# Performance work log

Hardware: AMD Instinct MI355X
Metric: run time of the kernel (lower is better)

Reference implementation:

```python
import jax, jax.numpy as jnp
import numpy as np

B, I, D = 2048, 20000, 512  # batch, nr_items, embedding_dim
EPS = 1e-12  # tf.nn.l2_normalize epsilon


def setup_inputs() -> dict:
    key = jax.random.key(0)
    ks = jax.random.split(key, 16)
    g = lambda k, shape, fan_in: jax.random.normal(k, shape, jnp.float32) * (1.0 / np.sqrt(fan_in))
    likes = (jax.random.uniform(ks[0], (B, I)) < 0.05).astype(jnp.float32)
    noise_mask = jax.random.uniform(ks[1], (B, I)) < 0.3
    users = jax.random.randint(ks[2], (B,), 0, 100000)
    return {
        'users': users, 'likes': likes, 'noise_mask': noise_mask,
        # encoder: I -> 2D (relu) -> D (relu)
        'enc_w1': g(ks[3], (I, 2 * D), I), 'enc_b1': jnp.zeros((2 * D,), jnp.float32),
        'enc_w2': g(ks[4], (2 * D, D), 2 * D), 'enc_b2': jnp.zeros((D,), jnp.float32),
        # likes_estimator: D -> 2D (relu) -> I (sigmoid)
        'lk_w1': g(ks[5], (D, 2 * D), D), 'lk_b1': jnp.zeros((2 * D,), jnp.float32),
        'lk_w2': g(ks[6], (2 * D, I), 2 * D), 'lk_b2': jnp.zeros((I,), jnp.float32),
        # rec_estimator: D -> 2D (relu) -> I (sigmoid)
        'rc_w1': g(ks[7], (D, 2 * D), D), 'rc_b1': jnp.zeros((2 * D,), jnp.float32),
        'rc_w2': g(ks[8], (2 * D, I), 2 * D), 'rc_b2': jnp.zeros((I,), jnp.float32),
    }


def reference(users, likes, noise_mask, enc_w1, enc_b1, enc_w2, enc_b2,
              lk_w1, lk_b1, lk_w2, lk_b2, rc_w1, rc_b1, rc_w2, rc_b2):
    noisy_likes = jnp.where(noise_mask, 0.0, likes)
    # encoder MLP
    h = jax.nn.relu(noisy_likes @ enc_w1 + enc_b1)
    embed_user = jax.nn.relu(h @ enc_w2 + enc_b2)          # [B, D]
    # heads
    estimated_likes = jax.nn.sigmoid(jax.nn.relu(embed_user @ lk_w1 + lk_b1) @ lk_w2 + lk_b2)
    estimated_rec = jax.nn.sigmoid(jax.nn.relu(embed_user @ rc_w1 + rc_b1) @ rc_w2 + rc_b2)
    # all-pairs cosine similarity as a Gram matrix (no NxNxD tile).
    # tf.keras.losses.cosine_similarity returns the NEGATIVE cosine similarity.
    normed = embed_user * jax.lax.rsqrt(
        jnp.maximum(jnp.sum(embed_user * embed_user, axis=-1, keepdims=True), EPS))
    user_sim = -(normed @ normed.T)                        # [B, B]
    popular = jnp.mean(likes, axis=0)                      # [I]
    return (estimated_likes, user_sim, estimated_rec, popular)
```

## Files before the change

kernel.cpp:

```cpp
#include <hip/hip_runtime.h>
#include <cstdint>
#include <cstddef>

#define B_DIM 2048
#define I_DIM 20000
#define D_DIM 512
#define H_DIM 1024

typedef __bf16 bf16x8 __attribute__((ext_vector_type(8)));
typedef float f32x4 __attribute__((ext_vector_type(4)));

__device__ __forceinline__ unsigned short f2bf(float f) {
  union { float f; unsigned u; } v; v.f = f;
  unsigned u = v.u;
  u += 0x7fffu + ((u >> 16) & 1u);
  return (unsigned short)(u >> 16);
}
__device__ __forceinline__ float bf2f(unsigned short h) {
  union { unsigned u; float f; } v; v.u = ((unsigned)h) << 16;
  return v.f;
}

__device__ __forceinline__ void glds16(const unsigned short* g, unsigned short* l) {
  __builtin_amdgcn_global_load_lds(
      (const __attribute__((address_space(1))) void*)g,
      (__attribute__((address_space(3))) void*)l, 16, 0, 0);
}

__global__ void noisy_popular_kernel(const float* __restrict__ likes,
                                     const int* __restrict__ mask,
                                     unsigned short* __restrict__ noisy,
                                     float* __restrict__ pop) {
  int idx4 = blockIdx.x * 256 + threadIdx.x;
  if (idx4 >= I_DIM / 4) return;
  int r0 = blockIdx.y * 64;
  float4 s = make_float4(0.f, 0.f, 0.f, 0.f);
  for (int r = 0; r < 64; ++r) {
    size_t off = (size_t)(r0 + r) * (I_DIM / 4) + idx4;
    float4 L = ((const float4*)likes)[off];
    int4 M = ((const int4*)mask)[off];
    s.x += L.x; s.y += L.y; s.z += L.z; s.w += L.w;
    ushort4 o;
    o.x = M.x ? (unsigned short)0 : f2bf(L.x);
    o.y = M.y ? (unsigned short)0 : f2bf(L.y);
    o.z = M.z ? (unsigned short)0 : f2bf(L.z);
    o.w = M.w ? (unsigned short)0 : f2bf(L.w);
    ((ushort4*)noisy)[off] = o;
  }
  const float inv = 1.0f / B_DIM;
  atomicAdd(&pop[idx4 * 4 + 0], s.x * inv);
  atomicAdd(&pop[idx4 * 4 + 1], s.y * inv);
  atomicAdd(&pop[idx4 * 4 + 2], s.z * inv);
  atomicAdd(&pop[idx4 * 4 + 3], s.w * inv);
}

__global__ void transpose_to_bf16(const float* __restrict__ in,
                                  unsigned short* __restrict__ out, int R, int C) {
  __shared__ unsigned short tile[32][33];
  int c0 = blockIdx.x * 32, r0 = blockIdx.y * 32;
  int tx = threadIdx.x, ty = threadIdx.y;
#pragma unroll
  for (int i = 0; i < 4; i++) {
    int r = r0 + ty + i * 8;
    tile[ty + i * 8][tx] = f2bf(in[(size_t)r * C + c0 + tx]);
  }
  __syncthreads();
#pragma unroll
  for (int i = 0; i < 4; i++) {
    int c = c0 + ty + i * 8;
    out[(size_t)c * R + r0 + tx] = tile[tx][ty + i * 8];
  }
}

__global__ void concat_bias_kernel(const float* __restrict__ a,
                                   const float* __restrict__ b,
                                   float* __restrict__ out) {
  int i = blockIdx.x * 256 + threadIdx.x;
  if (i < H_DIM) out[i] = a[i];
  else if (i < 2 * H_DIM) out[i] = b[i - H_DIM];
}

__global__ void reduce_relu_kernel(const float* __restrict__ partial,
                                   const float* __restrict__ bias,
                                   unsigned short* __restrict__ h1) {
  int idx4 = blockIdx.x * 256 + threadIdx.x;
  const size_t slice = (size_t)B_DIM * H_DIM / 4;
  float4 s = ((const float4*)partial)[idx4];
#pragma unroll
  for (int z = 1; z < 5; z++) {
    float4 p = ((const float4*)partial)[z * slice + idx4];
    s.x += p.x; s.y += p.y; s.z += p.z; s.w += p.w;
  }
  float4 b = ((const float4*)bias)[idx4 & (H_DIM / 4 - 1)];
  ushort4 o;
  o.x = f2bf(fmaxf(s.x + b.x, 0.f));
  o.y = f2bf(fmaxf(s.y + b.y, 0.f));
  o.z = f2bf(fmaxf(s.z + b.z, 0.f));
  o.w = f2bf(fmaxf(s.w + b.w, 0.f));
  ((ushort4*)h1)[idx4] = o;
}

__global__ void l2norm_kernel(const unsigned short* __restrict__ embed,
                              unsigned short* __restrict__ normed) {
  int row = blockIdx.x * 4 + (threadIdx.x >> 6);
  int lane = threadIdx.x & 63;
  const unsigned short* e = embed + (size_t)row * D_DIM;
  float v[8];
  float ss = 0.f;
#pragma unroll
  for (int j = 0; j < 8; j++) { v[j] = bf2f(e[lane + j * 64]); ss += v[j] * v[j]; }
#pragma unroll
  for (int o = 32; o > 0; o >>= 1) ss += __shfl_xor(ss, o, 64);
  float s = rsqrtf(fmaxf(ss, 1e-12f));
  unsigned short* nr = normed + (size_t)row * D_DIM;
#pragma unroll
  for (int j = 0; j < 8; j++) nr[lane + j * 64] = f2bf(v[j] * s);
}

template <int ACT, bool OBF16>
__global__ __launch_bounds__(256) void gemm128(
    const unsigned short* __restrict__ A, const unsigned short* __restrict__ BT,
    const float* __restrict__ bias, void* __restrict__ Cout,
    int N, int lda, int ldb, int ldc, int kLen, long long zStride) {
  __shared__ unsigned short As[128 * 32];
  __shared__ unsigned short Bs[128 * 32];
  const int n0 = blockIdx.x * 128;
  const int m0 = blockIdx.y * 128;
  const int t = threadIdx.x;
  const int lane = t & 63;
  const int wv = t >> 6;
  const int quad = lane >> 4;
  const int tc = lane & 15;
  const int wm = (wv >> 1) * 64;
  const int wn = (wv & 1) * 64;
  const int k0 = blockIdx.z * kLen;

  f32x4 acc[4][4];
#pragma unroll
  for (int i = 0; i < 4; i++)
#pragma unroll
    for (int j = 0; j < 4; j++) acc[i][j] = (f32x4){0.f, 0.f, 0.f, 0.f};

  const int srow = lane >> 2;
  const int skch = (lane & 3) * 8;
  const unsigned short* gA0 = A + (size_t)(m0 + wv * 32 + srow) * lda + k0 + skch;
  const unsigned short* gA1 = gA0 + (size_t)16 * lda;
  const unsigned short* gB0 = BT + (size_t)(n0 + wv * 32 + srow) * ldb + k0 + skch;
  const unsigned short* gB1 = gB0 + (size_t)16 * ldb;
  unsigned short* lA = As + wv * 1024;
  unsigned short* lB = Bs + wv * 1024;

  const int nIter = kLen >> 5;
  for (int it = 0; it < nIter; ++it) {
    __syncthreads();
    glds16(gA0, lA);
    glds16(gA1, lA + 512);
    glds16(gB0, lB);
    glds16(gB1, lB + 512);
    gA0 += 32; gA1 += 32; gB0 += 32; gB1 += 32;
    __syncthreads();
    bf16x8 a[4], b[4];
#pragma unroll
    for (int i = 0; i < 4; i++) {
      a[i] = *(const bf16x8*)&As[(wm + i * 16 + tc) * 32 + quad * 8];
      b[i] = *(const bf16x8*)&Bs[(wn + i * 16 + tc) * 32 + quad * 8];
    }
#pragma unroll
    for (int i = 0; i < 4; i++)
#pragma unroll
      for (int j = 0; j < 4; j++)
        acc[i][j] =
            __builtin_amdgcn_mfma_f32_16x16x32_bf16(a[i], b[j], acc[i][j], 0, 0, 0);
  }

  float* outF = (float*)Cout + (size_t)blockIdx.z * zStride;
  unsigned short* outH = (unsigned short*)Cout;
#pragma unroll
  for (int j = 0; j < 4; j++) {
    int col = n0 + wn + j * 16 + tc;
    if (col >= N) continue;
    float bv = bias ? bias[col] : 0.f;
#pragma unroll
    for (int i = 0; i < 4; i++) {
      int row0 = m0 + wm + i * 16 + quad * 4;
#pragma unroll
      for (int r = 0; r < 4; r++) {
        float v = acc[i][j][r] + bv;
        if (ACT == 1) v = fmaxf(v, 0.f);
        else if (ACT == 2) v = 1.f / (1.f + __expf(-v));
        else if (ACT == 3) v = -v;
        if (OBF16)
          outH[(size_t)(row0 + r) * ldc + col] = f2bf(v);
        else
          outF[(size_t)(row0 + r) * ldc + col] = v;
      }
    }
  }
}

extern "C" void kernel_launch(void* const* d_in, const int* in_sizes, int n_in,
                              void* d_out, int out_size, void* d_ws, size_t ws_size,
                              hipStream_t stream) {
  const float* likes = (const float*)d_in[1];
  const int* mask = (const int*)d_in[2];
  const float* enc_w1 = (const float*)d_in[3];
  const float* enc_b1 = (const float*)d_in[4];
  const float* enc_w2 = (const float*)d_in[5];
  const float* enc_b2 = (const float*)d_in[6];
  const float* lk_w1 = (const float*)d_in[7];
  const float* lk_b1 = (const float*)d_in[8];
  const float* lk_w2 = (const float*)d_in[9];
  const float* lk_b2 = (const float*)d_in[10];
  const float* rc_w1 = (const float*)d_in[11];
  const float* rc_b1 = (const float*)d_in[12];
  const float* rc_w2 = (const float*)d_in[13];
  const float* rc_b2 = (const float*)d_in[14];

  float* out_likes = (float*)d_out;
  float* out_sim = out_likes + (size_t)B_DIM * I_DIM;
  float* out_rec = out_sim + (size_t)B_DIM * B_DIM;
  float* out_pop = out_rec + (size_t)B_DIM * I_DIM;

  unsigned short* ws = (unsigned short*)d_ws;
  unsigned short* A_noisy = ws;
  unsigned short* LK2T = ws;
  unsigned short* RC2T = ws + 20578304;
  unsigned short* W1T = ws + 41156608;
  unsigned short* W2T = W1T + 20480000;
  unsigned short* W1catT = W2T + 524288;
  float* bcat = (float*)(W1catT + 1048576);
  unsigned short* h1 = W1catT + 1048576 + 4096;
  unsigned short* hboth = h1 + 2097152;
  unsigned short* embed = hboth + 4194304;
  unsigned short* normed = embed + 1048576;
  float* partial = out_rec;

  hipMemsetAsync(out_pop, 0, I_DIM * sizeof(float), stream);
  noisy_popular_kernel<<<dim3((I_DIM / 4 + 255) / 256, B_DIM / 64), 256, 0,
                         stream>>>(likes, mask, A_noisy, out_pop);

  transpose_to_bf16<<<dim3(H_DIM / 32, I_DIM / 32), dim3(32, 8), 0, stream>>>(
      enc_w1, W1T, I_DIM, H_DIM);
  gemm128<0, false><<<dim3(H_DIM / 128, B_DIM / 128, 5), 256, 0, stream>>>(
      A_noisy, W1T, nullptr, partial, H_DIM, I_DIM, I_DIM, H_DIM, 4000,
      (long long)B_DIM * H_DIM);
  reduce_relu_kernel<<<B_DIM * H_DIM / 4 / 256, 256, 0, stream>>>(partial, enc_b1,
                                                                  h1);

  transpose_to_bf16<<<dim3(D_DIM / 32, H_DIM / 32), dim3(32, 8), 0, stream>>>(
      enc_w2, W2T, H_DIM, D_DIM);
  gemm128<1, true><<<dim3(D_DIM / 128, B_DIM / 128, 1), 256, 0, stream>>>(
      h1, W2T, enc_b2, embed, D_DIM, H_DIM, H_DIM, D_DIM, H_DIM, 0);

  l2norm_kernel<<<B_DIM / 4, 256, 0, stream>>>(embed, normed);
  gemm128<3, false><<<dim3(B_DIM / 128, B_DIM / 128, 1), 256, 0, stream>>>(
      normed, normed, nullptr, out_sim, B_DIM, D_DIM, D_DIM, B_DIM, D_DIM, 0);

  concat_bias_kernel<<<2 * H_DIM / 256, 256, 0, stream>>>(lk_b1, rc_b1, bcat);
  transpose_to_bf16<<<dim3(H_DIM / 32, D_DIM / 32), dim3(32, 8), 0, stream>>>(
      lk_w1, W1catT, D_DIM, H_DIM);
  transpose_to_bf16<<<dim3(H_DIM / 32, D_DIM / 32), dim3(32, 8), 0, stream>>>(
      rc_w1, W1catT + (size_t)H_DIM * D_DIM, D_DIM, H_DIM);
  gemm128<1, true><<<dim3(2 * H_DIM / 128, B_DIM / 128, 1), 256, 0, stream>>>(
      embed, W1catT, bcat, hboth, 2 * H_DIM, D_DIM, D_DIM, 2 * H_DIM, D_DIM, 0);

  transpose_to_bf16<<<dim3(I_DIM / 32, H_DIM / 32), dim3(32, 8), 0, stream>>>(
      lk_w2, LK2T, H_DIM, I_DIM);
  transpose_to_bf16<<<dim3(I_DIM / 32, H_DIM / 32), dim3(32, 8), 0, stream>>>(
      rc_w2, RC2T, H_DIM, I_DIM);
  gemm128<2, false><<<dim3((I_DIM + 127) / 128, B_DIM / 128, 1), 256, 0, stream>>>(
      hboth, LK2T, lk_b2, out_likes, I_DIM, 2 * H_DIM, H_DIM, I_DIM, H_DIM, 0);
  gemm128<2, false><<<dim3((I_DIM + 127) / 128, B_DIM / 128, 1), 256, 0, stream>>>(
      hboth + H_DIM, RC2T, rc_b2, out_rec, I_DIM, 2 * H_DIM, H_DIM, I_DIM, H_DIM, 0);
}
```

Before: 1.284 ms.

## Add 256x256 pipelined MFMA GEMM for encoder and output heads with padded K

Introduces a 512-thread gemm256 kernel with 256x256 tiles, double-buffered LDS staged through global_load_lds, a swizzled layout, and interleaved read/MFMA phases that use setprio. It replaces gemm128 for the large encoder GEMM, which now has K padded to 20480 and is split 8 ways, and for both 20000-wide output heads. The aim is more data reuse per tile and better overlap of loads with MFMA work. In exchange it uses 128KB of dynamic LDS, which limits occupancy. Padding adds zero-fill writes, and the head grid is only 79x8 blocks.

```diff
diff --git a/kernel.cpp b/kernel.cpp
--- a/kernel.cpp
+++ b/kernel.cpp
@@ -4,6 +4,8 @@
 
 #define B_DIM 2048
 #define I_DIM 20000
+#define IPAD 20480
+#define NPAD 20224
 #define D_DIM 512
 #define H_DIM 1024
 
@@ -32,20 +34,25 @@
                                      unsigned short* __restrict__ noisy,
                                      float* __restrict__ pop) {
   int idx4 = blockIdx.x * 256 + threadIdx.x;
-  if (idx4 >= I_DIM / 4) return;
   int r0 = blockIdx.y * 64;
+  if (idx4 >= I_DIM / 4) {
+    ushort4 z = make_ushort4(0, 0, 0, 0);
+    for (int r = 0; r < 64; ++r)
+      ((ushort4*)noisy)[(size_t)(r0 + r) * (IPAD / 4) + idx4] = z;
+    return;
+  }
   float4 s = make_float4(0.f, 0.f, 0.f, 0.f);
   for (int r = 0; r < 64; ++r) {
-    size_t off = (size_t)(r0 + r) * (I_DIM / 4) + idx4;
-    float4 L = ((const float4*)likes)[off];
-    int4 M = ((const int4*)mask)[off];
+    size_t inoff = (size_t)(r0 + r) * (I_DIM / 4) + idx4;
+    float4 L = ((const float4*)likes)[inoff];
+    int4 M = ((const int4*)mask)[inoff];
     s.x += L.x; s.y += L.y; s.z += L.z; s.w += L.w;
     ushort4 o;
     o.x = M.x ? (unsigned short)0 : f2bf(L.x);
     o.y = M.y ? (unsigned short)0 : f2bf(L.y);
     o.z = M.z ? (unsigned short)0 : f2bf(L.z);
     o.w = M.w ? (unsigned short)0 : f2bf(L.w);
-    ((ushort4*)noisy)[off] = o;
+    ((ushort4*)noisy)[(size_t)(r0 + r) * (IPAD / 4) + idx4] = o;
   }
   const float inv = 1.0f / B_DIM;
   atomicAdd(&pop[idx4 * 4 + 0], s.x * inv);
@@ -55,20 +62,22 @@
 }
 
 __global__ void transpose_to_bf16(const float* __restrict__ in,
-                                  unsigned short* __restrict__ out, int R, int C) {
+                                  unsigned short* __restrict__ out, int Rpad,
+                                  int C, int Rvalid) {
   __shared__ unsigned short tile[32][33];
   int c0 = blockIdx.x * 32, r0 = blockIdx.y * 32;
   int tx = threadIdx.x, ty = threadIdx.y;
 #pragma unroll
   for (int i = 0; i < 4; i++) {
     int r = r0 + ty + i * 8;
-    tile[ty + i * 8][tx] = f2bf(in[(size_t)r * C + c0 + tx]);
+    tile[ty + i * 8][tx] =
+        (r < Rvalid) ? f2bf(in[(size_t)r * C + c0 + tx]) : (unsigned short)0;
   }
   __syncthreads();
 #pragma unroll
   for (int i = 0; i < 4; i++) {
     int c = c0 + ty + i * 8;
-    out[(size_t)c * R + r0 + tx] = tile[tx][ty + i * 8];
+    out[(size_t)c * Rpad + r0 + tx] = tile[tx][ty + i * 8];
   }
 }
 
@@ -80,6 +89,7 @@
   else if (i < 2 * H_DIM) out[i] = b[i - H_DIM];
 }
 
+template <int Z>
 __global__ void reduce_relu_kernel(const float* __restrict__ partial,
                                    const float* __restrict__ bias,
                                    unsigned short* __restrict__ h1) {
@@ -87,7 +97,7 @@
   const size_t slice = (size_t)B_DIM * H_DIM / 4;
   float4 s = ((const float4*)partial)[idx4];
 #pragma unroll
-  for (int z = 1; z < 5; z++) {
+  for (int z = 1; z < Z; z++) {
     float4 p = ((const float4*)partial)[z * slice + idx4];
     s.x += p.x; s.y += p.y; s.z += p.z; s.w += p.w;
   }
@@ -198,6 +208,174 @@
   }
 }
 
+template <int ACT, bool OBF16>
+__global__ __launch_bounds__(512, 2) void gemm256(
+    const unsigned short* __restrict__ A, const unsigned short* __restrict__ BT,
+    const float* __restrict__ bias, void* __restrict__ Cout,
+    int N, int lda, int ldb, int ldc, int kLen, long long zStride) {
+  extern __shared__ unsigned short lds[];
+  const int n0 = blockIdx.x * 256;
+  const int m0 = blockIdx.y * 256;
+  const int t = threadIdx.x;
+  const int L = t & 63;
+  const int w = t >> 6;
+  const int quad = L >> 4;
+  const int tc = L & 15;
+  const int wm = (w >> 2) * 128;
+  const int wn = (w & 3) * 64;
+  const int k0 = blockIdx.z * kLen;
+
+  const int srow = L >> 3;
+  const int scol = ((L & 7) ^ srow) * 8;
+  size_t aOff[2][2], bOff[2][2];
+#pragma unroll
+  for (int h = 0; h < 2; h++)
+#pragma unroll
+    for (int c = 0; c < 2; c++) {
+      aOff[h][c] = (size_t)(m0 + h * 128 + w * 16 + c * 8 + srow) * lda + k0 + scol;
+      bOff[h][c] = (size_t)(n0 + h * 128 + w * 16 + c * 8 + srow) * ldb + k0 + scol;
+    }
+  const int stageW = w * 1024;
+  const int BO1 = 32768;
+
+  const int aR0 = (wm >> 7) * 8192;
+  const int aR1 = BO1 + aR0;
+  const int bR0 = 16384 + (wn >> 7) * 8192;
+  const int bR1 = BO1 + bR0;
+  const int swz = (tc & 7) << 3;
+
+  f32x4 acc[8][4];
+#pragma unroll
+  for (int i = 0; i < 8; i++)
+#pragma unroll
+    for (int j = 0; j < 4; j++) acc[i][j] = (f32x4){0.f, 0.f, 0.f, 0.f};
+
+  bf16x8 aF[4][2], bF0[2][2], bF1[2][2];
+
+#define STAGE_A(h, kt, bo)                                                        \
+  do {                                                                            \
+    glds16(A + aOff[h][0] + (size_t)(kt) * 64, lds + (bo) + (h) * 8192 + stageW); \
+    glds16(A + aOff[h][1] + (size_t)(kt) * 64,                                    \
+           lds + (bo) + (h) * 8192 + stageW + 512);                               \
+  } while (0)
+#define STAGE_B(h, kt, bo)                                                        \
+  do {                                                                            \
+    glds16(BT + bOff[h][0] + (size_t)(kt) * 64,                                   \
+           lds + (bo) + 16384 + (h) * 8192 + stageW);                             \
+    glds16(BT + bOff[h][1] + (size_t)(kt) * 64,                                   \
+           lds + (bo) + 16384 + (h) * 8192 + stageW + 512);                       \
+  } while (0)
+
+  auto RD_A = [&](int base, int i0) {
+#pragma unroll
+    for (int ii = 0; ii < 4; ii++) {
+      const int row = (i0 + ii) * 16 + tc;
+#pragma unroll
+      for (int ks = 0; ks < 2; ks++)
+        aF[ii][ks] =
+            *(const bf16x8*)&lds[base + row * 64 + (((ks * 4 + quad) * 8) ^ swz)];
+    }
+  };
+  auto RD_B = [&](int base, int jg, bf16x8(&bF)[2][2]) {
+#pragma unroll
+    for (int jj = 0; jj < 2; jj++) {
+      const int row = (wn & 64) + (jg * 2 + jj) * 16 + tc;
+#pragma unroll
+      for (int ks = 0; ks < 2; ks++)
+        bF[jj][ks] =
+            *(const bf16x8*)&lds[base + row * 64 + (((ks * 4 + quad) * 8) ^ swz)];
+    }
+  };
+  auto MM = [&](int ig, bf16x8(&bF)[2][2], int jg) {
+#pragma unroll
+    for (int ii = 0; ii < 4; ii++)
+#pragma unroll
+      for (int jj = 0; jj < 2; jj++)
+#pragma unroll
+        for (int ks = 0; ks < 2; ks++)
+          acc[ig * 4 + ii][jg * 2 + jj] = __builtin_amdgcn_mfma_f32_16x16x32_bf16(
+              aF[ii][ks], bF[jj][ks], acc[ig * 4 + ii][jg * 2 + jj], 0, 0, 0);
+  };
+
+#define PH_MID()                                      \
+  __builtin_amdgcn_s_barrier();                       \
+  asm volatile("s_waitcnt lgkmcnt(0)" ::: "memory");  \
+  __builtin_amdgcn_sched_barrier(0);                  \
+  __builtin_amdgcn_s_setprio(1)
+#define PH_END()                                      \
+  __builtin_amdgcn_s_setprio(0);                      \
+  __builtin_amdgcn_sched_barrier(0);                  \
+  __builtin_amdgcn_s_barrier()
+#define VMW4() asm volatile("s_waitcnt vmcnt(4)" ::: "memory")
+
+  const int nT = kLen >> 6;
+  const int nIt = nT >> 1;
+
+  STAGE_A(0, 0, 0); STAGE_A(1, 0, 0); STAGE_B(0, 0, 0); STAGE_B(1, 0, 0);
+  STAGE_B(0, 1, BO1); STAGE_B(1, 1, BO1);
+  VMW4();
+  __builtin_amdgcn_s_barrier();
+
+#pragma unroll 1
+  for (int it = 0; it < nIt; ++it) {
+    const int T = it << 1;
+    const int ktA1 = T + 1;
+    const int kt2 = (T + 2 < nT) ? T + 2 : nT - 1;
+    const int kt3 = (T + 3 < nT) ? T + 3 : nT - 1;
+    RD_A(aR0, 0); RD_B(bR0, 0, bF0);
+    STAGE_A(0, ktA1, BO1);
+    PH_MID(); MM(0, bF0, 0); PH_END();
+    RD_B(bR0, 1, bF1);
+    STAGE_A(1, ktA1, BO1);
+    PH_MID(); MM(0, bF1, 1); PH_END();
+    RD_A(aR0, 4);
+    STAGE_B(0, kt2, 0);
+    PH_MID(); MM(1, bF0, 0); PH_END();
+    STAGE_B(1, kt2, 0);
+    PH_MID(); MM(1, bF1, 1); VMW4(); PH_END();
+    RD_A(aR1, 0); RD_B(bR1, 0, bF0);
+    STAGE_A(0, kt2, 0);
+    PH_MID(); MM(0, bF0, 0); PH_END();
+    RD_B(bR1, 1, bF1);
+    STAGE_A(1, kt2, 0);
+    PH_MID(); MM(0, bF1, 1); PH_END();
+    RD_A(aR1, 4);
+    STAGE_B(0, kt3, BO1);
+    PH_MID(); MM(1, bF0, 0); PH_END();
+    STAGE_B(1, kt3, BO1);
+    PH_MID(); MM(1, bF1, 1); VMW4(); PH_END();
+  }
+#undef STAGE_A
+#undef STAGE_B
+#undef PH_MID
+#undef PH_END
+#undef VMW4
+
+  float* outF = (float*)Cout + (size_t)blockIdx.z * zStride;
+  unsigned short* outH = (unsigned short*)Cout;
+#pragma unroll
+  for (int j = 0; j < 4; j++) {
+    const int col = n0 + wn + j * 16 + tc;
+    if (col >= N) continue;
+    const float bv = bias ? bias[col] : 0.f;
+#pragma unroll
+    for (int i = 0; i < 8; i++) {
+      const int row0 = m0 + wm + i * 16 + quad * 4;
+#pragma unroll
+      for (int r = 0; r < 4; r++) {
+        float v = acc[i][j][r] + bv;
+        if (ACT == 1) v = fmaxf(v, 0.f);
+        else if (ACT == 2) v = 1.f / (1.f + __expf(-v));
+        else if (ACT == 3) v = -v;
+        if (OBF16)
+          outH[(size_t)(row0 + r) * ldc + col] = f2bf(v);
+        else
+          outF[(size_t)(row0 + r) * ldc + col] = v;
+      }
+    }
+  }
+}
+
 extern "C" void kernel_launch(void* const* d_in, const int* in_sizes, int n_in,
                               void* d_out, int out_size, void* d_ws, size_t ws_size,
                               hipStream_t stream) {
@@ -224,31 +402,40 @@
   unsigned short* ws = (unsigned short*)d_ws;
   unsigned short* A_noisy = ws;
   unsigned short* LK2T = ws;
-  unsigned short* RC2T = ws + 20578304;
-  unsigned short* W1T = ws + 41156608;
-  unsigned short* W2T = W1T + 20480000;
-  unsigned short* W1catT = W2T + 524288;
-  float* bcat = (float*)(W1catT + 1048576);
-  unsigned short* h1 = W1catT + 1048576 + 4096;
-  unsigned short* hboth = h1 + 2097152;
-  unsigned short* embed = hboth + 4194304;
-  unsigned short* normed = embed + 1048576;
+  unsigned short* RC2T = ws + (size_t)NPAD * H_DIM;
+  unsigned short* W1T = ws + (size_t)B_DIM * IPAD;
+  unsigned short* W2T = W1T + (size_t)H_DIM * IPAD;
+  unsigned short* W1catT = W2T + (size_t)D_DIM * H_DIM;
+  float* bcat = (float*)(W1catT + (size_t)2 * H_DIM * D_DIM);
+  unsigned short* h1 = W1catT + (size_t)2 * H_DIM * D_DIM + 2 * H_DIM * 2;
+  unsigned short* hboth = h1 + (size_t)B_DIM * H_DIM;
+  unsigned short* embed = hboth + (size_t)B_DIM * 2 * H_DIM;
+  unsigned short* normed = embed + (size_t)B_DIM * D_DIM;
   float* partial = out_rec;
 
+  static bool attrDone = false;
+  if (!attrDone) {
+    (void)hipFuncSetAttribute(reinterpret_cast<const void*>(&gemm256<0, false>),
+                              hipFuncAttributeMaxDynamicSharedMemorySize, 131072);
+    (void)hipFuncSetAttribute(reinterpret_cast<const void*>(&gemm256<2, false>),
+                              hipFuncAttributeMaxDynamicSharedMemorySize, 131072);
+    attrDone = true;
+  }
+
   hipMemsetAsync(out_pop, 0, I_DIM * sizeof(float), stream);
-  noisy_popular_kernel<<<dim3((I_DIM / 4 + 255) / 256, B_DIM / 64), 256, 0,
-                         stream>>>(likes, mask, A_noisy, out_pop);
-
-  transpose_to_bf16<<<dim3(H_DIM / 32, I_DIM / 32), dim3(32, 8), 0, stream>>>(
-      enc_w1, W1T, I_DIM, H_DIM);
-  gemm128<0, false><<<dim3(H_DIM / 128, B_DIM / 128, 5), 256, 0, stream>>>(
-      A_noisy, W1T, nullptr, partial, H_DIM, I_DIM, I_DIM, H_DIM, 4000,
+  noisy_popular_kernel<<<dim3(IPAD / 4 / 256, B_DIM / 64), 256, 0, stream>>>(
+      likes, mask, A_noisy, out_pop);
+
+  transpose_to_bf16<<<dim3(H_DIM / 32, IPAD / 32), dim3(32, 8), 0, stream>>>(
+      enc_w1, W1T, IPAD, H_DIM, I_DIM);
+  gemm256<0, false><<<dim3(H_DIM / 256, B_DIM / 256, 8), 512, 131072, stream>>>(
+      A_noisy, W1T, nullptr, partial, H_DIM, IPAD, IPAD, H_DIM, IPAD / 8,
       (long long)B_DIM * H_DIM);
-  reduce_relu_kernel<<<B_DIM * H_DIM / 4 / 256, 256, 0, stream>>>(partial, enc_b1,
-                                                                  h1);
+  reduce_relu_kernel<8><<<B_DIM * H_DIM / 4 / 256, 256, 0, stream>>>(partial,
+                                                                     enc_b1, h1);
 
   transpose_to_bf16<<<dim3(D_DIM / 32, H_DIM / 32), dim3(32, 8), 0, stream>>>(
-      enc_w2, W2T, H_DIM, D_DIM);
+      enc_w2, W2T, H_DIM, D_DIM, H_DIM);
   gemm128<1, true><<<dim3(D_DIM / 128, B_DIM / 128, 1), 256, 0, stream>>>(
       h1, W2T, enc_b2, embed, D_DIM, H_DIM, H_DIM, D_DIM, H_DIM, 0);
 
@@ -258,18 +445,18 @@
 
   concat_bias_kernel<<<2 * H_DIM / 256, 256, 0, stream>>>(lk_b1, rc_b1, bcat);
   transpose_to_bf16<<<dim3(H_DIM / 32, D_DIM / 32), dim3(32, 8), 0, stream>>>(
-      lk_w1, W1catT, D_DIM, H_DIM);
+      lk_w1, W1catT, D_DIM, H_DIM, D_DIM);
   transpose_to_bf16<<<dim3(H_DIM / 32, D_DIM / 32), dim3(32, 8), 0, stream>>>(
-      rc_w1, W1catT + (size_t)H_DIM * D_DIM, D_DIM, H_DIM);
+      rc_w1, W1catT + (size_t)H_DIM * D_DIM, D_DIM, H_DIM, D_DIM);
   gemm128<1, true><<<dim3(2 * H_DIM / 128, B_DIM / 128, 1), 256, 0, stream>>>(
       embed, W1catT, bcat, hboth, 2 * H_DIM, D_DIM, D_DIM, 2 * H_DIM, D_DIM, 0);
 
   transpose_to_bf16<<<dim3(I_DIM / 32, H_DIM / 32), dim3(32, 8), 0, stream>>>(
-      lk_w2, LK2T, H_DIM, I_DIM);
+      lk_w2, LK2T, H_DIM, I_DIM, H_DIM);
   transpose_to_bf16<<<dim3(I_DIM / 32, H_DIM / 32), dim3(32, 8), 0, stream>>>(
-      rc_w2, RC2T, H_DIM, I_DIM);
-  gemm128<2, false><<<dim3((I_DIM + 127) / 128, B_DIM / 128, 1), 256, 0, stream>>>(
+      rc_w2, RC2T, H_DIM, I_DIM, H_DIM);
+  gemm256<2, false><<<dim3(NPAD / 256, B_DIM / 256, 1), 512, 131072, stream>>>(
       hboth, LK2T, lk_b2, out_likes, I_DIM, 2 * H_DIM, H_DIM, I_DIM, H_DIM, 0);
-  gemm128<2, false><<<dim3((I_DIM + 127) / 128, B_DIM / 128, 1), 256, 0, stream>>>(
+  gemm256<2, false><<<dim3(NPAD / 256, B_DIM / 256, 1), 512, 131072, stream>>>(
       hboth + H_DIM, RC2T, rc_b2, out_rec, I_DIM, 2 * H_DIM, H_DIM, I_DIM, H_DIM, 0);
 }
```

Result: faster. 1.164 ms (-9.3%).
